# Kernel tuning notes

Measured on AMD Instinct MI355X. Metric: run time of the kernel, lower is better.

## Reference

```python
import jax, jax.numpy as jnp
import numpy as np

B, L, D = 2, 2048, 1024
H = 16
DH = D // H
DFF = 4096
THETA = 10000.0
EPS = 1e-5


def setup_inputs() -> dict:
    key = jax.random.key(0)
    ks = jax.random.split(key, 6)
    s_qkv = (2.0 / (D + 3 * D)) ** 0.5
    s_o = (2.0 / (D + D)) ** 0.5
    s_ff = (2.0 / (D + DFF)) ** 0.5
    return {
        'x': jax.random.normal(ks[0], (B, L, D), jnp.float32),
        'w_qkv': jax.random.normal(ks[1], (3 * D, D), jnp.float32) * s_qkv,
        'w_o': jax.random.normal(ks[2], (D, D), jnp.float32) * s_o,
        'w1': jax.random.normal(ks[3], (DFF, D), jnp.float32) * s_ff,
        'w2': jax.random.normal(ks[4], (D, DFF), jnp.float32) * s_ff,
        'w3': jax.random.normal(ks[5], (DFF, D), jnp.float32) * s_ff,
        'g1': jnp.ones((D,), jnp.float32),
        'g2': jnp.ones((D,), jnp.float32),
    }


def _rmsnorm(x, g):
    xf = x.astype(jnp.float32)
    inv = jax.lax.rsqrt(jnp.mean(xf * xf, axis=-1, keepdims=True) + EPS)
    return (xf * inv * g).astype(x.dtype)


def _rotate_pair(t):
    # interleaved pairs: (x0,x1,x2,x3,...) -> (-x1,x0,-x3,x2,...)
    t2 = t.reshape(t.shape[:-1] + (t.shape[-1] // 2, 2))
    r = jnp.stack((-t2[..., 1], t2[..., 0]), axis=-1)
    return r.reshape(t.shape)


def reference(x, w_qkv, w_o, w1, w2, w3, g1, g2):
    Bb, Ll, Dd = x.shape
    # --- attention sublayer ---
    y = _rmsnorm(x, g1)
    qkv = y @ w_qkv.T                       # (B, L, 3D)
    q, k, v = jnp.split(qkv, 3, axis=-1)
    def to_heads(t):
        return t.reshape(Bb, Ll, H, DH).transpose(0, 2, 1, 3)  # (B,H,L,Dh)
    q, k, v = to_heads(q), to_heads(k), to_heads(v)
    # RoPE (interleaved), positions = 0..L-1
    inv_freq = 1.0 / (THETA ** (jnp.arange(0, DH, 2, dtype=jnp.float32) / DH))
    ang = jnp.arange(Ll, dtype=jnp.float32)[:, None] * inv_freq  # (L, Dh/2)
    ang = jnp.repeat(ang, 2, axis=-1)                            # (L, Dh)
    cos, sin = jnp.cos(ang), jnp.sin(ang)
    q = q * cos + _rotate_pair(q) * sin
    k = k * cos + _rotate_pair(k) * sin
    att = jnp.einsum('bhqd,bhkd->bhqk', q, k) * (1.0 / np.sqrt(DH))
    causal = jnp.tril(jnp.ones((Ll, Ll), dtype=bool))
    att = jnp.where(causal, att, -jnp.inf)
    att = jax.nn.softmax(att, axis=-1)
    yh = jnp.einsum('bhqk,bhkd->bhqd', att, v)
    y = yh.transpose(0, 2, 1, 3).reshape(Bb, Ll, Dd)
    x = x + y @ w_o.T
    # --- SwiGLU FFN sublayer ---
    y = _rmsnorm(x, g2)
    h = jax.nn.silu(y @ w1.T) * (y @ w3.T)
    return x + h @ w2.T
```

## Files before the change

kernel.cpp:

```cpp
#include <hip/hip_runtime.h>


typedef __attribute__((ext_vector_type(8))) short short8;
typedef __attribute__((ext_vector_type(4))) float f32x4;

#define DEV __device__ __forceinline__

DEV unsigned short f2b(float f) {
  unsigned int u = __builtin_bit_cast(unsigned int, f);
  unsigned int r = u + 0x7fffu + ((u >> 16) & 1u);
  return (unsigned short)(r >> 16);
}
DEV float b2f(unsigned short h) {
  return __builtin_bit_cast(float, ((unsigned int)h) << 16);
}
DEV unsigned int cvtpk(float lo, float hi) {
  unsigned int r;
  asm("v_cvt_pk_bf16_f32 %0, %1, %2" : "=v"(r) : "v"(lo), "v"(hi));
  return r;
}
DEV f32x4 MFMA(short8 a, short8 b, f32x4 c) {
  return __builtin_amdgcn_mfma_f32_16x16x32_bf16(a, b, c, 0, 0, 0);
}
DEV void gload16(const void* g, void* lds) {
  __builtin_amdgcn_global_load_lds((const __attribute__((address_space(1))) void*)g,
                                   (__attribute__((address_space(3))) void*)lds, 16, 0, 0);
}

__global__ __launch_bounds__(256) void prep_k(
    const float* __restrict__ wqkv, const float* __restrict__ wo,
    const float* __restrict__ w1, const float* __restrict__ w3,
    const float* __restrict__ w2,
    unsigned short* __restrict__ wqkv_b, unsigned short* __restrict__ wo_b,
    unsigned short* __restrict__ w1_b, unsigned short* __restrict__ w3_b,
    unsigned short* __restrict__ w2_b,
    float2* __restrict__ rtab,
    const float* __restrict__ x, const float* __restrict__ g1,
    unsigned short* __restrict__ yb) {
  const int bid = blockIdx.x;
  const int t = threadIdx.x;
  if (bid < 16384) {
    const float* src;
    unsigned short* dst;
    int base;
    if (bid < 3072) { src = wqkv; dst = wqkv_b; base = bid; }
    else if (bid < 4096) { src = wo; dst = wo_b; base = bid - 3072; }
    else if (bid < 8192) { src = w1; dst = w1_b; base = bid - 4096; }
    else if (bid < 12288) { src = w3; dst = w3_b; base = bid - 8192; }
    else { src = w2; dst = w2_b; base = bid - 12288; }
    const int i = (base * 256 + t) * 4;
    float4 v = *(const float4*)(src + i);
    ushort4 o;
    o.x = f2b(v.x); o.y = f2b(v.y); o.z = f2b(v.z); o.w = f2b(v.w);
    *(ushort4*)(dst + i) = o;
  } else if (bid < 16640) {
    const int i = (bid - 16384) * 256 + t;
    const int lt = i >> 5, pr = i & 31;
    const float invf = __expf((float)pr * -0.28782313662425572f);
    const float ang = (float)lt * invf;
    float sn, cs;
    sincosf(ang, &sn, &cs);
    rtab[i] = make_float2(cs, sn);
  } else {
    const int row = bid - 16640;
    const float4 v = *(const float4*)(x + (size_t)row * 1024 + t * 4);
    float ss = v.x * v.x + v.y * v.y + v.z * v.z + v.w * v.w;
#pragma unroll
    for (int m = 32; m >= 1; m >>= 1) ss += __shfl_xor(ss, m, 64);
    __shared__ float red[4];
    if ((t & 63) == 0) red[t >> 6] = ss;
    __syncthreads();
    float tot = red[0] + red[1] + red[2] + red[3];
    float inv = rsqrtf(tot * (1.0f / 1024.0f) + 1e-5f);
    ushort4 o;
    o.x = f2b(v.x * inv * g1[t * 4 + 0]);
    o.y = f2b(v.y * inv * g1[t * 4 + 1]);
    o.z = f2b(v.z * inv * g1[t * 4 + 2]);
    o.w = f2b(v.w * inv * g1[t * 4 + 3]);
    *(ushort4*)(yb + (size_t)row * 1024 + t * 4) = o;
  }
}

__global__ __launch_bounds__(256) void rms_k(const float* __restrict__ x,
                                             const float* __restrict__ g,
                                             unsigned short* __restrict__ out) {
  const int row = blockIdx.x;
  const int t = threadIdx.x;
  const float4 v = *(const float4*)(x + (size_t)row * 1024 + t * 4);
  float ss = v.x * v.x + v.y * v.y + v.z * v.z + v.w * v.w;
#pragma unroll
  for (int m = 32; m >= 1; m >>= 1) ss += __shfl_xor(ss, m, 64);
  __shared__ float red[4];
  if ((t & 63) == 0) red[t >> 6] = ss;
  __syncthreads();
  float tot = red[0] + red[1] + red[2] + red[3];
  float inv = rsqrtf(tot * (1.0f / 1024.0f) + 1e-5f);
  ushort4 o;
  o.x = f2b(v.x * inv * g[t * 4 + 0]);
  o.y = f2b(v.y * inv * g[t * 4 + 1]);
  o.z = f2b(v.z * inv * g[t * 4 + 2]);
  o.w = f2b(v.w * inv * g[t * 4 + 3]);
  *(ushort4*)(out + (size_t)row * 1024 + t * 4) = o;
}

template <int MODE>
__global__ __launch_bounds__(256, 3) void gemm_bt(
    const unsigned short* __restrict__ A, const unsigned short* __restrict__ B0,
    int M, int N, int K,
    float* __restrict__ outF, const float* __restrict__ resid,
    unsigned short* __restrict__ q, unsigned short* __restrict__ k2,
    unsigned short* __restrict__ v,
    const float2* __restrict__ rtab) {
  __shared__ __align__(16) unsigned short As[2][128 * 32];
  __shared__ __align__(16) unsigned short Bs[2][128 * 32];
  const int t = threadIdx.x;
  const int wv = t >> 6, ln = t & 63;
  const int l15 = ln & 15, grp = ln >> 4;
  const int wr = wv >> 1, wc = wv & 1;
  int m0, n0;
  if constexpr (MODE == 1) {
    const int d = blockIdx.y * 8 + blockIdx.x;
    const int xcd = d & 7, j = d >> 3;
    m0 = (xcd * 4 + (j >> 3)) * 128;
    n0 = (j & 7) * 128;
  } else {
    m0 = blockIdx.y * 128;
    n0 = blockIdx.x * 128;
  }

  const char* sA0 = (const char*)A + ((size_t)(m0 + (t >> 2)) * K + (t & 3) * 8) * 2;
  const char* sA1 = (const char*)A + ((size_t)(m0 + 64 + (t >> 2)) * K + (t & 3) * 8) * 2;
  const char* sB0 = (const char*)B0 + ((size_t)(n0 + (t >> 2)) * K + (t & 3) * 8) * 2;
  const char* sB1 = (const char*)B0 + ((size_t)(n0 + 64 + (t >> 2)) * K + (t & 3) * 8) * 2;

  f32x4 acc[4][4];
#pragma unroll
  for (int mm = 0; mm < 4; ++mm)
#pragma unroll
    for (int nn = 0; nn < 4; ++nn) acc[mm][nn] = (f32x4){0.f, 0.f, 0.f, 0.f};

  const int KT = K >> 5;
  gload16(sA0, (char*)As[0] + wv * 1024);
  gload16(sA1, (char*)As[0] + 4096 + wv * 1024);
  gload16(sB0, (char*)Bs[0] + wv * 1024);
  gload16(sB1, (char*)Bs[0] + 4096 + wv * 1024);

#pragma unroll 1
  for (int kt = 0; kt < KT; ++kt) {
    const int par = kt & 1;
    const size_t ko = (size_t)((kt + 1 < KT) ? (kt + 1) : kt) * 64;
    gload16(sA0 + ko, (char*)As[par ^ 1] + wv * 1024);
    gload16(sA1 + ko, (char*)As[par ^ 1] + 4096 + wv * 1024);
    gload16(sB0 + ko, (char*)Bs[par ^ 1] + wv * 1024);
    gload16(sB1 + ko, (char*)Bs[par ^ 1] + 4096 + wv * 1024);
    asm volatile("s_waitcnt vmcnt(4)" ::: "memory");
    __builtin_amdgcn_s_barrier();
    const unsigned short* Ab = As[par];
    const unsigned short* Bb = Bs[par];
    short8 af[4], bf0[4];
#pragma unroll
    for (int mm = 0; mm < 4; ++mm)
      af[mm] = *(const short8*)&Ab[(wr * 64 + mm * 16 + l15) * 32 + grp * 8];
#pragma unroll
    for (int nn = 0; nn < 4; ++nn)
      bf0[nn] = *(const short8*)&Bb[(wc * 64 + nn * 16 + l15) * 32 + grp * 8];
#pragma unroll
    for (int mm = 0; mm < 4; ++mm)
#pragma unroll
      for (int nn = 0; nn < 4; ++nn) acc[mm][nn] = MFMA(af[mm], bf0[nn], acc[mm][nn]);
    __builtin_amdgcn_s_barrier();
  }

#pragma unroll
  for (int mm = 0; mm < 4; ++mm)
#pragma unroll
    for (int nn = 0; nn < 4; ++nn)
#pragma unroll
      for (int j = 0; j < 4; ++j) {
        const int r = m0 + wr * 64 + mm * 16 + grp * 4 + j;
        const int c = n0 + wc * 64 + nn * 16 + l15;
        float val = acc[mm][nn][j];
        if constexpr (MODE == 0) {
          const int mat = c >> 10;
          const int rem = c & 1023;
          const int hh = rem >> 6;
          const int dh = rem & 63;
          const int bt = r >> 11;
          const int lt = r & 2047;
          float outv = val;
          if (mat < 2) {
            const float partner = __shfl_xor(val, 1, 64);
            const float2 cs = rtab[lt * 32 + (dh >> 1)];
            outv = (dh & 1) ? (val * cs.x + partner * cs.y) : (val * cs.x - partner * cs.y);
          }
          if (mat == 0) outv *= 0.18033688011112042f;
          unsigned short* dst = (mat == 0) ? q : ((mat == 1) ? k2 : v);
          dst[((size_t)(bt * 16 + hh) * 2048 + lt) * 64 + dh] = f2b(outv);
        } else {
          const size_t idx = (size_t)r * N + c;
          outF[idx] = resid[idx] + val;
        }
      }
}

__global__ __launch_bounds__(256, 3) void gemm_sk(
    const unsigned short* __restrict__ A, const unsigned short* __restrict__ B0,
    unsigned short* __restrict__ part) {
  __shared__ __align__(16) unsigned short As[2][128 * 32];
  __shared__ __align__(16) unsigned short Bs[2][128 * 32];
  const int t = threadIdx.x;
  const int wv = t >> 6, ln = t & 63;
  const int l15 = ln & 15, grp = ln >> 4;
  const int wr = wv >> 1, wc = wv & 1;
  const int d = blockIdx.y * 8 + blockIdx.x;
  const int xcd = d & 7, j = d >> 3;
  const int m0 = (xcd * 4 + (j >> 3)) * 128;
  const int n0 = (j & 7) * 128;
  const size_t kbase = (size_t)blockIdx.z * 2048;

  const char* sA0 = (const char*)A + ((size_t)(m0 + (t >> 2)) * 4096 + kbase + (t & 3) * 8) * 2;
  const char* sA1 = (const char*)A + ((size_t)(m0 + 64 + (t >> 2)) * 4096 + kbase + (t & 3) * 8) * 2;
  const char* sB0 = (const char*)B0 + ((size_t)(n0 + (t >> 2)) * 4096 + kbase + (t & 3) * 8) * 2;
  const char* sB1 = (const char*)B0 + ((size_t)(n0 + 64 + (t >> 2)) * 4096 + kbase + (t & 3) * 8) * 2;

  f32x4 acc[4][4];
#pragma unroll
  for (int mm = 0; mm < 4; ++mm)
#pragma unroll
    for (int nn = 0; nn < 4; ++nn) acc[mm][nn] = (f32x4){0.f, 0.f, 0.f, 0.f};

  gload16(sA0, (char*)As[0] + wv * 1024);
  gload16(sA1, (char*)As[0] + 4096 + wv * 1024);
  gload16(sB0, (char*)Bs[0] + wv * 1024);
  gload16(sB1, (char*)Bs[0] + 4096 + wv * 1024);

#pragma unroll 1
  for (int kt = 0; kt < 64; ++kt) {
    const int par = kt & 1;
    const size_t ko = (size_t)((kt + 1 < 64) ? (kt + 1) : kt) * 64;
    gload16(sA0 + ko, (char*)As[par ^ 1] + wv * 1024);
    gload16(sA1 + ko, (char*)As[par ^ 1] + 4096 + wv * 1024);
    gload16(sB0 + ko, (char*)Bs[par ^ 1] + wv * 1024);
    gload16(sB1 + ko, (char*)Bs[par ^ 1] + 4096 + wv * 1024);
    asm volatile("s_waitcnt vmcnt(4)" ::: "memory");
    __builtin_amdgcn_s_barrier();
    const unsigned short* Ab = As[par];
    const unsigned short* Bb = Bs[par];
    short8 af[4], bf0[4];
#pragma unroll
    for (int mm = 0; mm < 4; ++mm)
      af[mm] = *(const short8*)&Ab[(wr * 64 + mm * 16 + l15) * 32 + grp * 8];
#pragma unroll
    for (int nn = 0; nn < 4; ++nn)
      bf0[nn] = *(const short8*)&Bb[(wc * 64 + nn * 16 + l15) * 32 + grp * 8];
#pragma unroll
    for (int mm = 0; mm < 4; ++mm)
#pragma unroll
      for (int nn = 0; nn < 4; ++nn) acc[mm][nn] = MFMA(af[mm], bf0[nn], acc[mm][nn]);
    __builtin_amdgcn_s_barrier();
  }

  unsigned short* pz = part + (size_t)blockIdx.z * 4194304;
#pragma unroll
  for (int mm = 0; mm < 4; ++mm)
#pragma unroll
    for (int nn = 0; nn < 4; ++nn)
#pragma unroll
      for (int j = 0; j < 4; ++j) {
        const int r = m0 + wr * 64 + mm * 16 + grp * 4 + j;
        const int c = n0 + wc * 64 + nn * 16 + l15;
        pz[(size_t)r * 1024 + c] = f2b(acc[mm][nn][j]);
      }
}

__global__ __launch_bounds__(256) void red_k(const float* __restrict__ x2,
                                             const unsigned short* __restrict__ part,
                                             float* __restrict__ out) {
  const int i = (blockIdx.x * 256 + threadIdx.x) * 4;
  float4 r = *(const float4*)(x2 + i);
#pragma unroll
  for (int z = 0; z < 2; ++z) {
    const ushort4 p = *(const ushort4*)(part + (size_t)z * 4194304 + i);
    r.x += b2f(p.x);
    r.y += b2f(p.y);
    r.z += b2f(p.z);
    r.w += b2f(p.w);
  }
  *(float4*)(out + i) = r;
}

__global__ __launch_bounds__(512, 2) void ffn_k(
    const unsigned short* __restrict__ A, const unsigned short* __restrict__ B0,
    const unsigned short* __restrict__ B1, unsigned short* __restrict__ outH) {
  __shared__ __align__(16) char Asm[2][32768];
  __shared__ __align__(16) char Bsm[2][32768];
  const int t = threadIdx.x;
  const int wid = t >> 6, lane = t & 63;
  const int l15 = lane & 15, grp = lane >> 4;
  const int wr = wid >> 2, wc = wid & 3;
  const int d = blockIdx.x;
  const int xcd = d & 7, r8 = d >> 3;
  const int m0 = (r8 >> 2) * 256;
  const int n0 = (xcd * 4 + (r8 & 3)) * 256;

  const char* srcA0;
  const char* srcB0;
  {
    const int lb = t * 16;
    const int r = lb >> 7;
    const int sw = (((lb >> 4) & 7) * 16) ^ ((r & 7) << 4);
    srcA0 = (const char*)A + (size_t)(m0 + r) * 2048 + sw;
    const int R = n0 + r;
    const unsigned short* bsrc = ((R >> 4) & 1) ? B1 : B0;
    const int br = ((R >> 5) << 4) + (R & 15);
    srcB0 = (const char*)bsrc + (size_t)br * 2048 + sw;
  }
  char* const ldsA = (char*)Asm + wid * 1024;
  char* const ldsB = (char*)Bsm + wid * 1024;

  f32x4 acc[8][4];
#pragma unroll
  for (int m = 0; m < 8; ++m)
#pragma unroll
    for (int n = 0; n < 4; ++n) acc[m][n] = (f32x4){0.f, 0.f, 0.f, 0.f};

  gload16(srcA0 + 0 * 131072, ldsA + 0 * 8192);
  gload16(srcA0 + 1 * 131072, ldsA + 1 * 8192);
  gload16(srcB0 + 0 * 65536, ldsB + 0 * 8192);
  gload16(srcB0 + 1 * 65536, ldsB + 1 * 8192);
  gload16(srcB0 + 2 * 65536, ldsB + 2 * 8192);
  gload16(srcB0 + 3 * 65536, ldsB + 3 * 8192);
  gload16(srcA0 + 2 * 131072, ldsA + 2 * 8192);
  gload16(srcA0 + 3 * 131072, ldsA + 3 * 8192);

  const int rA0 = wr * 64 + l15;
  const int rB0 = wc * 32 + l15;

#pragma unroll 1
  for (int kt = 0; kt < 16; ++kt) {
    const int cb = kt & 1;
    const size_t koff = (size_t)((kt + 1 < 16) ? (kt + 1) : kt) * 128;
    const char* Ab = Asm[cb];
    const char* Bb = Bsm[cb];
    const int nb = (cb ^ 1) * 32768;

    short8 a0[2][4], a1[2][4], b0[2][2], b1[2][2];

    gload16(srcA0 + 0 * 131072 + koff, ldsA + nb + 0 * 8192);
    gload16(srcA0 + 1 * 131072 + koff, ldsA + nb + 1 * 8192);
    asm volatile("s_waitcnt vmcnt(4)" ::: "memory");
    __builtin_amdgcn_s_barrier();
#pragma unroll
    for (int ks = 0; ks < 2; ++ks)
#pragma unroll
      for (int m = 0; m < 4; ++m) {
        const int r = rA0 + m * 16;
        a0[ks][m] = *(const short8*)(Ab + r * 128 + ((ks * 64 + grp * 16) ^ ((r & 7) << 4)));
      }
#pragma unroll
    for (int ks = 0; ks < 2; ++ks)
#pragma unroll
      for (int n = 0; n < 2; ++n) {
        const int r = rB0 + n * 16;
        b0[ks][n] = *(const short8*)(Bb + r * 128 + ((ks * 64 + grp * 16) ^ ((r & 7) << 4)));
      }
#pragma unroll
    for (int ks = 0; ks < 2; ++ks)
#pragma unroll
      for (int n = 0; n < 2; ++n) {
        const int r = 128 + rB0 + n * 16;
        b1[ks][n] = *(const short8*)(Bb + r * 128 + ((ks * 64 + grp * 16) ^ ((r & 7) << 4)));
      }
    __builtin_amdgcn_s_setprio(1);
#pragma unroll
    for (int ks = 0; ks < 2; ++ks)
#pragma unroll
      for (int m = 0; m < 4; ++m)
#pragma unroll
        for (int n = 0; n < 2; ++n) acc[m][n] = MFMA(a0[ks][m], b0[ks][n], acc[m][n]);
    __builtin_amdgcn_s_setprio(0);

    gload16(srcB0 + 0 * 65536 + koff, ldsB + nb + 0 * 8192);
    gload16(srcB0 + 1 * 65536 + koff, ldsB + nb + 1 * 8192);
    gload16(srcB0 + 2 * 65536 + koff, ldsB + nb + 2 * 8192);
    gload16(srcB0 + 3 * 65536 + koff, ldsB + nb + 3 * 8192);
    asm volatile("s_waitcnt vmcnt(6)" ::: "memory");
    __builtin_amdgcn_s_barrier();
#pragma unroll
    for (int ks = 0; ks < 2; ++ks)
#pragma unroll
      for (int m = 0; m < 4; ++m) {
        const int r = 128 + rA0 + m * 16;
        a1[ks][m] = *(const short8*)(Ab + r * 128 + ((ks * 64 + grp * 16) ^ ((r & 7) << 4)));
      }
    __builtin_amdgcn_s_setprio(1);
#pragma unroll
    for (int ks = 0; ks < 2; ++ks)
#pragma unroll
      for (int m = 0; m < 4; ++m)
#pragma unroll
        for (int n = 0; n < 2; ++n) acc[m][2 + n] = MFMA(a0[ks][m], b1[ks][n], acc[m][2 + n]);
    __builtin_amdgcn_s_setprio(0);

    gload16(srcA0 + 2 * 131072 + koff, ldsA + nb + 2 * 8192);
    gload16(srcA0 + 3 * 131072 + koff, ldsA + nb + 3 * 8192);
    __builtin_amdgcn_s_barrier();
    __builtin_amdgcn_s_setprio(1);
#pragma unroll
    for (int ks = 0; ks < 2; ++ks)
#pragma unroll
      for (int m = 0; m < 4; ++m)
#pragma unroll
        for (int n = 0; n < 2; ++n) acc[4 + m][2 + n] = MFMA(a1[ks][m], b1[ks][n], acc[4 + m][2 + n]);
    __builtin_amdgcn_s_setprio(0);

    __builtin_amdgcn_s_barrier();
    __builtin_amdgcn_s_setprio(1);
#pragma unroll
    for (int ks = 0; ks < 2; ++ks)
#pragma unroll
      for (int m = 0; m < 4; ++m)
#pragma unroll
        for (int n = 0; n < 2; ++n) acc[4 + m][n] = MFMA(a1[ks][m], b0[ks][n], acc[4 + m][n]);
    __builtin_amdgcn_s_setprio(0);
  }

#pragma unroll
  for (int mh = 0; mh < 2; ++mh)
#pragma unroll
    for (int m = 0; m < 4; ++m)
#pragma unroll
      for (int nh = 0; nh < 2; ++nh)
#pragma unroll
        for (int j = 0; j < 4; ++j) {
          const int row = m0 + mh * 128 + wr * 64 + m * 16 + grp * 4 + j;
          const int ch = (n0 >> 1) + nh * 64 + wc * 16 + l15;
          const float a1v = acc[mh * 4 + m][nh * 2 + 0][j];
          const float a3v = acc[mh * 4 + m][nh * 2 + 1][j];
          const float hval = a1v / (1.0f + __expf(-a1v)) * a3v;
          outH[(size_t)row * 4096 + ch] = f2b(hval);
        }
}

__global__ __launch_bounds__(256) void vtr_k(const unsigned short* __restrict__ v,
                                             unsigned short* __restrict__ vt) {
  __shared__ __align__(16) unsigned short tile[64][72];
  const int bh = blockIdx.y;
  const int lt0 = blockIdx.x * 64;
  const int t = threadIdx.x;
  const int r = t >> 2;
  const int c0 = (t & 3) * 16;
  const unsigned short* src = v + ((size_t)bh * 2048 + lt0 + r) * 64 + c0;
  *(short8*)&tile[r][c0] = *(const short8*)src;
  *(short8*)&tile[r][c0 + 8] = *(const short8*)(src + 8);
  __syncthreads();
  unsigned short outv[16];
#pragma unroll
  for (int i = 0; i < 16; ++i) outv[i] = tile[c0 + i][r];
  unsigned short* dst = vt + ((size_t)bh * 64 + r) * 2048 + lt0 + c0;
  *(short8*)dst = *(short8*)&outv[0];
  *(short8*)(dst + 8) = *(short8*)&outv[8];
}

__global__ __launch_bounds__(256) void attn_k(const unsigned short* __restrict__ qb,
                                              const unsigned short* __restrict__ kb,
                                              const unsigned short* __restrict__ vt,
                                              unsigned short* __restrict__ yh) {
  const int dd = blockIdx.x;
  const int xcd = dd & 7, idx = dd >> 3;
  const int bh = xcd + 8 * (idx & 3);
  const int pair = idx >> 2;
  const int t = threadIdx.x;
  const int w = t >> 6, lane = t & 63;
  const int l15 = lane & 15, grp = lane >> 4;

  __shared__ __align__(16) char Ks[2][8192];
  __shared__ __align__(16) char Vs[2][8192];
  __shared__ __align__(16) char Ps[8192];
  char* Pw = Ps + w * 2048;

  const char* kg = (const char*)kb + (size_t)bh * 262144;
  const char* vg = (const char*)vt + (size_t)bh * 262144;

  const int lb0 = t * 16, lb1 = 4096 + t * 16;
  const int r0 = lb0 >> 7, r1 = lb1 >> 7;
  const int sl0 = (lb0 & 0x70) ^ ((r0 & 7) << 4);
  const int sl1 = (lb1 & 0x70) ^ ((r1 & 7) << 4);
  const char* srcK0 = kg + r0 * 128 + sl0;
  const char* srcK1 = kg + r1 * 128 + sl1;
  const char* srcV0 = vg + (size_t)r0 * 4096 + sl0;
  const char* srcV1 = vg + (size_t)r1 * 4096 + sl1;

  const int bq = bh >> 4, hh = bh & 15;

#pragma unroll 1
  for (int half = 0; half < 2; ++half) {
    const int qblk = half ? pair : (31 - pair);
    const int qw = qblk * 64 + w * 16;

    const unsigned short* qp = qb + ((size_t)bh * 2048 + qw) * 64;
    const short8 qf0 = *(const short8*)(qp + l15 * 64 + grp * 8);
    const short8 qf1 = *(const short8*)(qp + l15 * 64 + 32 + grp * 8);

    f32x4 o[4];
#pragma unroll
    for (int d = 0; d < 4; ++d) o[d] = (f32x4){0.f, 0.f, 0.f, 0.f};
    float mrun = -3.0e38f, lrun = 0.f;

    const int nkt = qblk + 1;

    __syncthreads();
    {
      gload16(srcK0, Ks[0] + w * 1024);
      gload16(srcK1, Ks[0] + 4096 + w * 1024);
      gload16(srcV0, Vs[0] + w * 1024);
      gload16(srcV1, Vs[0] + 4096 + w * 1024);
    }

#pragma unroll 1
    for (int kt = 0; kt < nkt; ++kt) {
      const int par = kt & 1;
      const int ktn = (kt + 1 < nkt) ? (kt + 1) : kt;
      gload16(srcK0 + (size_t)ktn * 8192, Ks[par ^ 1] + w * 1024);
      gload16(srcK1 + (size_t)ktn * 8192, Ks[par ^ 1] + 4096 + w * 1024);
      gload16(srcV0 + ktn * 128, Vs[par ^ 1] + w * 1024);
      gload16(srcV1 + ktn * 128, Vs[par ^ 1] + 4096 + w * 1024);
      asm volatile("s_waitcnt vmcnt(4)" ::: "memory");
      __builtin_amdgcn_s_barrier();

      const char* Kc = Ks[par];
      const char* Vc = Vs[par];

      f32x4 st[4];
#pragma unroll
      for (int c = 0; c < 4; ++c) {
        const int r = c * 16 + l15;
        const int xr = (r & 7) << 4;
        const short8 kf0 = *(const short8*)(Kc + r * 128 + ((grp * 16) ^ xr));
        const short8 kf1 = *(const short8*)(Kc + r * 128 + ((64 + grp * 16) ^ xr));
        f32x4 z = (f32x4){0.f, 0.f, 0.f, 0.f};
        __builtin_amdgcn_s_setprio(1);
        z = MFMA(kf0, qf0, z);
        z = MFMA(kf1, qf1, z);
        __builtin_amdgcn_s_setprio(0);
        st[c] = z;
      }

      const bool diag = (kt == qblk);
      const int qg = qw + l15;
      float av[4][4];
      float tm = -3.0e38f;
#pragma unroll
      for (int c = 0; c < 4; ++c)
#pragma unroll
        for (int j = 0; j < 4; ++j) {
          float x = st[c][j];
          if (diag) {
            const int kg2 = kt * 64 + c * 16 + grp * 4 + j;
            if (kg2 > qg) x = -3.0e38f;
          }
          av[c][j] = x;
          tm = fmaxf(tm, x);
        }
      tm = fmaxf(tm, __shfl_xor(tm, 16, 64));
      tm = fmaxf(tm, __shfl_xor(tm, 32, 64));

      const float mold = mrun;
      const bool need = tm > mold;
      mrun = fmaxf(mold, tm);
      const float aown = need ? __builtin_amdgcn_exp2f(mold - mrun) : 1.0f;
      if (__any(need)) {
        float am[4];
#pragma unroll
        for (int j = 0; j < 4; ++j) am[j] = __shfl(aown, grp * 4 + j, 64);
#pragma unroll
        for (int d = 0; d < 4; ++d)
#pragma unroll
          for (int j = 0; j < 4; ++j) o[d][j] *= am[j];
      }

      float rs = 0.f;
      uint2 pk[4];
#pragma unroll
      for (int c = 0; c < 4; ++c) {
        const float p0 = __builtin_amdgcn_exp2f(av[c][0] - mrun);
        const float p1 = __builtin_amdgcn_exp2f(av[c][1] - mrun);
        const float p2 = __builtin_amdgcn_exp2f(av[c][2] - mrun);
        const float p3 = __builtin_amdgcn_exp2f(av[c][3] - mrun);
        rs += (p0 + p1) + (p2 + p3);
        pk[c].x = cvtpk(p0, p1);
        pk[c].y = cvtpk(p2, p3);
      }
      rs += __shfl_xor(rs, 16, 64);
      rs += __shfl_xor(rs, 32, 64);
      lrun = lrun * aown + rs;

      const int xp = (l15 & 7) << 4;
      char* prow = Pw + l15 * 128;
#pragma unroll
      for (int c = 0; c < 4; ++c)
        *(uint2*)(prow + ((32 * c + 8 * grp) ^ xp)) = pk[c];

      const short8 pa0 = *(const short8*)(prow + ((grp * 16) ^ xp));
      const short8 pa1 = *(const short8*)(prow + ((64 + grp * 16) ^ xp));
#pragma unroll
      for (int db = 0; db < 4; ++db) {
        const int rv = db * 16 + l15;
        const int xv = (rv & 7) << 4;
        const short8 vf0 = *(const short8*)(Vc + rv * 128 + ((grp * 16) ^ xv));
        const short8 vf1 = *(const short8*)(Vc + rv * 128 + ((64 + grp * 16) ^ xv));
        __builtin_amdgcn_s_setprio(1);
        o[db] = MFMA(pa0, vf0, o[db]);
        o[db] = MFMA(pa1, vf1, o[db]);
        __builtin_amdgcn_s_setprio(0);
      }
      __builtin_amdgcn_s_barrier();
    }

    float lr[4];
#pragma unroll
    for (int j = 0; j < 4; ++j) lr[j] = __shfl(lrun, grp * 4 + j, 64);
#pragma unroll
    for (int db = 0; db < 4; ++db)
#pragma unroll
      for (int j = 0; j < 4; ++j) {
        const float valo = o[db][j] / lr[j];
        const size_t rowo = (size_t)bq * 2048 + qw + grp * 4 + j;
        yh[rowo * 1024 + hh * 64 + db * 16 + l15] = f2b(valo);
      }
  }
}

extern "C" void kernel_launch(void* const* d_in, const int* in_sizes, int n_in,
                              void* d_out, int out_size, void* d_ws, size_t ws_size,
                              hipStream_t stream) {
  const float* x = (const float*)d_in[0];
  const float* wqkv = (const float*)d_in[1];
  const float* wo = (const float*)d_in[2];
  const float* w1 = (const float*)d_in[3];
  const float* w2 = (const float*)d_in[4];
  const float* w3 = (const float*)d_in[5];
  const float* g1 = (const float*)d_in[6];
  const float* g2 = (const float*)d_in[7];

  char* ws = (char*)d_ws;
  unsigned short* wqkv_b = (unsigned short*)(ws + 0);
  unsigned short* wo_b = (unsigned short*)(ws + 6291456);
  unsigned short* w1_b = (unsigned short*)(ws + 8388608);
  unsigned short* w3_b = (unsigned short*)(ws + 16777216);
  unsigned short* yb = (unsigned short*)(ws + 25165824);
  float* x2 = (float*)(ws + 33554432);
  float2* rtab = (float2*)(ws + 33554432);
  unsigned short* w2_b = (unsigned short*)(ws + 50331648);
  unsigned short* qb = (unsigned short*)(ws + 58720256);
  unsigned short* kb = (unsigned short*)(ws + 67108864);
  unsigned short* vb = (unsigned short*)(ws + 75497472);
  unsigned short* vt = (unsigned short*)(ws + 83886080);
  unsigned short* yh = vb;
  unsigned short* hb = (unsigned short*)(ws + 58720256);
  unsigned short* part = (unsigned short*)(ws + 0);
  if (ws_size < 92274688) return;

  prep_k<<<20736, 256, 0, stream>>>(wqkv, wo, w1, w3, w2,
                                    wqkv_b, wo_b, w1_b, w3_b, w2_b,
                                    rtab, x, g1, yb);
  gemm_bt<0><<<dim3(24, 32), 256, 0, stream>>>(yb, wqkv_b, 4096, 3072, 1024,
                                               nullptr, nullptr, qb, kb, vb, rtab);
  vtr_k<<<dim3(32, 32), 256, 0, stream>>>(vb, vt);
  attn_k<<<dim3(512), 256, 0, stream>>>(qb, kb, vt, yh);
  gemm_bt<1><<<dim3(8, 32), 256, 0, stream>>>(yh, wo_b, 4096, 1024, 1024,
                                              x2, x, nullptr, nullptr, nullptr, nullptr);
  rms_k<<<4096, 256, 0, stream>>>(x2, g2, yb);
  ffn_k<<<dim3(512), 512, 0, stream>>>(yb, w1_b, w3_b, hb);
  gemm_sk<<<dim3(8, 32, 2), 256, 0, stream>>>(hb, w2_b, part);
  red_k<<<4096, 256, 0, stream>>>(x2, part, (float*)d_out);
}
```

Baseline: 272.0 us.

## Restructure FFN1 GEMM main loop into deeper ping-pong prefetch with unroll-by-two

Rewrites the gate/up GEMM K-loop as two K-tiles per iteration with fixed even and odd LDS buffers. Global-to-LDS loads for the tile two steps ahead are spread across the four MFMA quadrant phases, with more loads in flight (vmcnt 8). The aim is to hide global latency better and remove per-iteration buffer index arithmetic. In exchange it adds barriers around each phase, and the finer-grained buffer reuse raises the risk of synchronisation overhead or LDS write-after-read hazards.

```diff
diff --git a/kernel.cpp b/kernel.cpp
--- a/kernel.cpp
+++ b/kernel.cpp
@@ -332,44 +332,128 @@
   gload16(srcB0 + 3 * 65536, ldsB + 3 * 8192);
   gload16(srcA0 + 2 * 131072, ldsA + 2 * 8192);
   gload16(srcA0 + 3 * 131072, ldsA + 3 * 8192);
+  gload16(srcA0 + 0 * 131072 + 128, ldsA + 32768 + 0 * 8192);
+  gload16(srcA0 + 1 * 131072 + 128, ldsA + 32768 + 1 * 8192);
+  gload16(srcB0 + 0 * 65536 + 128, ldsB + 32768 + 0 * 8192);
+  gload16(srcB0 + 1 * 65536 + 128, ldsB + 32768 + 1 * 8192);
+  gload16(srcB0 + 2 * 65536 + 128, ldsB + 32768 + 2 * 8192);
+  gload16(srcB0 + 3 * 65536 + 128, ldsB + 32768 + 3 * 8192);
 
   const int rA0 = wr * 64 + l15;
   const int rB0 = wc * 32 + l15;
+  const char* const AbE = Asm[0];
+  const char* const BbE = Bsm[0];
+  const char* const AbO = Asm[1];
+  const char* const BbO = Bsm[1];
+
+  short8 a0[2][4], a1[2][4], b0[2][2], b1[2][2];
 
 #pragma unroll 1
-  for (int kt = 0; kt < 16; ++kt) {
-    const int cb = kt & 1;
-    const size_t koff = (size_t)((kt + 1 < 16) ? (kt + 1) : kt) * 128;
-    const char* Ab = Asm[cb];
-    const char* Bb = Bsm[cb];
-    const int nb = (cb ^ 1) * 32768;
-
-    short8 a0[2][4], a1[2][4], b0[2][2], b1[2][2];
-
-    gload16(srcA0 + 0 * 131072 + koff, ldsA + nb + 0 * 8192);
-    gload16(srcA0 + 1 * 131072 + koff, ldsA + nb + 1 * 8192);
-    asm volatile("s_waitcnt vmcnt(4)" ::: "memory");
+  for (int it = 0; it < 8; ++it) {
+    const size_t kO = (size_t)(2 * it + 1) * 128;
+    const int e2 = (2 * it + 2 < 16) ? (2 * it + 2) : 15;
+    const int o2 = (2 * it + 3 < 16) ? (2 * it + 3) : 15;
+    const size_t kE2 = (size_t)e2 * 128;
+    const size_t kO2 = (size_t)o2 * 128;
+
+    gload16(srcA0 + 2 * 131072 + kO, ldsA + 32768 + 2 * 8192);
+    gload16(srcA0 + 3 * 131072 + kO, ldsA + 32768 + 3 * 8192);
+    asm volatile("s_waitcnt vmcnt(8)" ::: "memory");
     __builtin_amdgcn_s_barrier();
 #pragma unroll
     for (int ks = 0; ks < 2; ++ks)
 #pragma unroll
       for (int m = 0; m < 4; ++m) {
         const int r = rA0 + m * 16;
-        a0[ks][m] = *(const short8*)(Ab + r * 128 + ((ks * 64 + grp * 16) ^ ((r & 7) << 4)));
+        a0[ks][m] = *(const short8*)(AbE + r * 128 + ((ks * 64 + grp * 16) ^ ((r & 7) << 4)));
       }
 #pragma unroll
     for (int ks = 0; ks < 2; ++ks)
 #pragma unroll
       for (int n = 0; n < 2; ++n) {
         const int r = rB0 + n * 16;
-        b0[ks][n] = *(const short8*)(Bb + r * 128 + ((ks * 64 + grp * 16) ^ ((r & 7) << 4)));
-      }
+        b0[ks][n] = *(const short8*)(BbE + r * 128 + ((ks * 64 + grp * 16) ^ ((r & 7) << 4)));
+      }
+    __builtin_amdgcn_s_setprio(1);
+#pragma unroll
+    for (int ks = 0; ks < 2; ++ks)
+#pragma unroll
+      for (int m = 0; m < 4; ++m)
+#pragma unroll
+        for (int n = 0; n < 2; ++n) acc[m][n] = MFMA(a0[ks][m], b0[ks][n], acc[m][n]);
+    __builtin_amdgcn_s_setprio(0);
+    __builtin_amdgcn_s_barrier();
+
 #pragma unroll
     for (int ks = 0; ks < 2; ++ks)
 #pragma unroll
       for (int n = 0; n < 2; ++n) {
         const int r = 128 + rB0 + n * 16;
-        b1[ks][n] = *(const short8*)(Bb + r * 128 + ((ks * 64 + grp * 16) ^ ((r & 7) << 4)));
+        b1[ks][n] = *(const short8*)(BbE + r * 128 + ((ks * 64 + grp * 16) ^ ((r & 7) << 4)));
+      }
+    gload16(srcA0 + 0 * 131072 + kE2, ldsA + 0 * 8192);
+    gload16(srcA0 + 1 * 131072 + kE2, ldsA + 1 * 8192);
+    __builtin_amdgcn_s_barrier();
+    __builtin_amdgcn_s_setprio(1);
+#pragma unroll
+    for (int ks = 0; ks < 2; ++ks)
+#pragma unroll
+      for (int m = 0; m < 4; ++m)
+#pragma unroll
+        for (int n = 0; n < 2; ++n) acc[m][2 + n] = MFMA(a0[ks][m], b1[ks][n], acc[m][2 + n]);
+    __builtin_amdgcn_s_setprio(0);
+    __builtin_amdgcn_s_barrier();
+
+#pragma unroll
+    for (int ks = 0; ks < 2; ++ks)
+#pragma unroll
+      for (int m = 0; m < 4; ++m) {
+        const int r = 128 + rA0 + m * 16;
+        a1[ks][m] = *(const short8*)(AbE + r * 128 + ((ks * 64 + grp * 16) ^ ((r & 7) << 4)));
+      }
+    gload16(srcB0 + 0 * 65536 + kE2, ldsB + 0 * 8192);
+    gload16(srcB0 + 1 * 65536 + kE2, ldsB + 1 * 8192);
+    __builtin_amdgcn_s_barrier();
+    __builtin_amdgcn_s_setprio(1);
+#pragma unroll
+    for (int ks = 0; ks < 2; ++ks)
+#pragma unroll
+      for (int m = 0; m < 4; ++m)
+#pragma unroll
+        for (int n = 0; n < 2; ++n) acc[4 + m][2 + n] = MFMA(a1[ks][m], b1[ks][n], acc[4 + m][2 + n]);
+    __builtin_amdgcn_s_setprio(0);
+    __builtin_amdgcn_s_barrier();
+
+    gload16(srcB0 + 2 * 65536 + kE2, ldsB + 2 * 8192);
+    gload16(srcB0 + 3 * 65536 + kE2, ldsB + 3 * 8192);
+    __builtin_amdgcn_s_barrier();
+    __builtin_amdgcn_s_setprio(1);
+#pragma unroll
+    for (int ks = 0; ks < 2; ++ks)
+#pragma unroll
+      for (int m = 0; m < 4; ++m)
+#pragma unroll
+        for (int n = 0; n < 2; ++n) acc[4 + m][n] = MFMA(a1[ks][m], b0[ks][n], acc[4 + m][n]);
+    __builtin_amdgcn_s_setprio(0);
+    __builtin_amdgcn_s_barrier();
+
+    gload16(srcA0 + 2 * 131072 + kE2, ldsA + 2 * 8192);
+    gload16(srcA0 + 3 * 131072 + kE2, ldsA + 3 * 8192);
+    asm volatile("s_waitcnt vmcnt(8)" ::: "memory");
+    __builtin_amdgcn_s_barrier();
+#pragma unroll
+    for (int ks = 0; ks < 2; ++ks)
+#pragma unroll
+      for (int m = 0; m < 4; ++m) {
+        const int r = rA0 + m * 16;
+        a0[ks][m] = *(const short8*)(AbO + r * 128 + ((ks * 64 + grp * 16) ^ ((r & 7) << 4)));
+      }
+#pragma unroll
+    for (int ks = 0; ks < 2; ++ks)
+#pragma unroll
+      for (int n = 0; n < 2; ++n) {
+        const int r = rB0 + n * 16;
+        b0[ks][n] = *(const short8*)(BbO + r * 128 + ((ks * 64 + grp * 16) ^ ((r & 7) << 4)));
       }
     __builtin_amdgcn_s_setprio(1);
 #pragma unroll
@@ -379,31 +463,37 @@
 #pragma unroll
         for (int n = 0; n < 2; ++n) acc[m][n] = MFMA(a0[ks][m], b0[ks][n], acc[m][n]);
     __builtin_amdgcn_s_setprio(0);
-
-    gload16(srcB0 + 0 * 65536 + koff, ldsB + nb + 0 * 8192);
-    gload16(srcB0 + 1 * 65536 + koff, ldsB + nb + 1 * 8192);
-    gload16(srcB0 + 2 * 65536 + koff, ldsB + nb + 2 * 8192);
-    gload16(srcB0 + 3 * 65536 + koff, ldsB + nb + 3 * 8192);
-    asm volatile("s_waitcnt vmcnt(6)" ::: "memory");
-    __builtin_amdgcn_s_barrier();
+    __builtin_amdgcn_s_barrier();
+
+#pragma unroll
+    for (int ks = 0; ks < 2; ++ks)
+#pragma unroll
+      for (int n = 0; n < 2; ++n) {
+        const int r = 128 + rB0 + n * 16;
+        b1[ks][n] = *(const short8*)(BbO + r * 128 + ((ks * 64 + grp * 16) ^ ((r & 7) << 4)));
+      }
+    gload16(srcA0 + 0 * 131072 + kO2, ldsA + 32768 + 0 * 8192);
+    gload16(srcA0 + 1 * 131072 + kO2, ldsA + 32768 + 1 * 8192);
+    __builtin_amdgcn_s_barrier();
+    __builtin_amdgcn_s_setprio(1);
+#pragma unroll
+    for (int ks = 0; ks < 2; ++ks)
+#pragma unroll
+      for (int m = 0; m < 4; ++m)
+#pragma unroll
+        for (int n = 0; n < 2; ++n) acc[m][2 + n] = MFMA(a0[ks][m], b1[ks][n], acc[m][2 + n]);
+    __builtin_amdgcn_s_setprio(0);
+    __builtin_amdgcn_s_barrier();
+
 #pragma unroll
     for (int ks = 0; ks < 2; ++ks)
 #pragma unroll
       for (int m = 0; m < 4; ++m) {
         const int r = 128 + rA0 + m * 16;
-        a1[ks][m] = *(const short8*)(Ab + r * 128 + ((ks * 64 + grp * 16) ^ ((r & 7) << 4)));
-      }
-    __builtin_amdgcn_s_setprio(1);
-#pragma unroll
-    for (int ks = 0; ks < 2; ++ks)
-#pragma unroll
-      for (int m = 0; m < 4; ++m)
-#pragma unroll
-        for (int n = 0; n < 2; ++n) acc[m][2 + n] = MFMA(a0[ks][m], b1[ks][n], acc[m][2 + n]);
-    __builtin_amdgcn_s_setprio(0);
-
-    gload16(srcA0 + 2 * 131072 + koff, ldsA + nb + 2 * 8192);
-    gload16(srcA0 + 3 * 131072 + koff, ldsA + nb + 3 * 8192);
+        a1[ks][m] = *(const short8*)(AbO + r * 128 + ((ks * 64 + grp * 16) ^ ((r & 7) << 4)));
+      }
+    gload16(srcB0 + 0 * 65536 + kO2, ldsB + 32768 + 0 * 8192);
+    gload16(srcB0 + 1 * 65536 + kO2, ldsB + 32768 + 1 * 8192);
     __builtin_amdgcn_s_barrier();
     __builtin_amdgcn_s_setprio(1);
 #pragma unroll
@@ -413,7 +503,10 @@
 #pragma unroll
         for (int n = 0; n < 2; ++n) acc[4 + m][2 + n] = MFMA(a1[ks][m], b1[ks][n], acc[4 + m][2 + n]);
     __builtin_amdgcn_s_setprio(0);
-
+    __builtin_amdgcn_s_barrier();
+
+    gload16(srcB0 + 2 * 65536 + kO2, ldsB + 32768 + 2 * 8192);
+    gload16(srcB0 + 3 * 65536 + kO2, ldsB + 32768 + 3 * 8192);
     __builtin_amdgcn_s_barrier();
     __builtin_amdgcn_s_setprio(1);
 #pragma unroll
@@ -423,6 +516,7 @@
 #pragma unroll
         for (int n = 0; n < 2; ++n) acc[4 + m][n] = MFMA(a1[ks][m], b0[ks][n], acc[4 + m][n]);
     __builtin_amdgcn_s_setprio(0);
+    __builtin_amdgcn_s_barrier();
   }
 
 #pragma unroll
```

After: 273.2 us. Within noise of the previous version (+0.5%).

## Double attention key tile to 128 and XCD-swizzle QKV GEMM grid

Applied to the files above, without the earlier changes.

The attention kernel now processes 128 keys per iteration instead of 64, using larger K/V/P shared-memory buffers and four MFMA k-steps for PV. This halves the number of loop iterations, barriers and online-softmax rescales. The causal mask is applied whenever the tile overlaps the diagonal, which wastes some work at the boundary. Separately, the QKV GEMM uses a 1D grid remapped so that blocks sharing A rows land on the same XCD, aiming for better L2 reuse. The larger LDS footprint may reduce occupancy.

```diff
diff --git a/kernel.cpp b/kernel.cpp
--- a/kernel.cpp
+++ b/kernel.cpp
@@ -124,8 +124,10 @@
     m0 = (xcd * 4 + (j >> 3)) * 128;
     n0 = (j & 7) * 128;
   } else {
-    m0 = blockIdx.y * 128;
-    n0 = blockIdx.x * 128;
+    const int d = blockIdx.x;
+    const int xcd = d & 7, qd = d >> 3;
+    m0 = (xcd + 8 * (qd / 24)) * 128;
+    n0 = (qd % 24) * 128;
   }
 
   const char* sA0 = (const char*)A + ((size_t)(m0 + (t >> 2)) * K + (t & 3) * 8) * 2;
@@ -474,22 +476,26 @@
   const int w = t >> 6, lane = t & 63;
   const int l15 = lane & 15, grp = lane >> 4;
 
-  __shared__ __align__(16) char Ks[2][8192];
-  __shared__ __align__(16) char Vs[2][8192];
-  __shared__ __align__(16) char Ps[8192];
-  char* Pw = Ps + w * 2048;
+  __shared__ __align__(16) char Ks[2][16384];
+  __shared__ __align__(16) char Vs[2][16384];
+  __shared__ __align__(16) char Ps[16384];
+  char* Pw = Ps + w * 4096;
 
   const char* kg = (const char*)kb + (size_t)bh * 262144;
   const char* vg = (const char*)vt + (size_t)bh * 262144;
 
-  const int lb0 = t * 16, lb1 = 4096 + t * 16;
-  const int r0 = lb0 >> 7, r1 = lb1 >> 7;
-  const int sl0 = (lb0 & 0x70) ^ ((r0 & 7) << 4);
-  const int sl1 = (lb1 & 0x70) ^ ((r1 & 7) << 4);
-  const char* srcK0 = kg + r0 * 128 + sl0;
-  const char* srcK1 = kg + r1 * 128 + sl1;
-  const char* srcV0 = vg + (size_t)r0 * 4096 + sl0;
-  const char* srcV1 = vg + (size_t)r1 * 4096 + sl1;
+  const char* srcK[4];
+  const char* srcV[4];
+#pragma unroll
+  for (int s = 0; s < 4; ++s) {
+    const int lb = s * 4096 + t * 16;
+    const int rK = lb >> 7;
+    const int oK = (lb & 0x70) ^ ((rK & 7) << 4);
+    srcK[s] = kg + rK * 128 + oK;
+    const int rV = lb >> 8;
+    const int oV = (lb & 0xF0) ^ ((rV & 7) << 4);
+    srcV[s] = vg + (size_t)rV * 4096 + oV;
+  }
 
   const int bq = bh >> 4, hh = bh & 15;
 
@@ -507,33 +513,33 @@
     for (int d = 0; d < 4; ++d) o[d] = (f32x4){0.f, 0.f, 0.f, 0.f};
     float mrun = -3.0e38f, lrun = 0.f;
 
-    const int nkt = qblk + 1;
+    const int nkt = (qblk + 2) >> 1;
 
     __syncthreads();
-    {
-      gload16(srcK0, Ks[0] + w * 1024);
-      gload16(srcK1, Ks[0] + 4096 + w * 1024);
-      gload16(srcV0, Vs[0] + w * 1024);
-      gload16(srcV1, Vs[0] + 4096 + w * 1024);
+#pragma unroll
+    for (int s = 0; s < 4; ++s) {
+      gload16(srcK[s], Ks[0] + s * 4096 + w * 1024);
+      gload16(srcV[s], Vs[0] + s * 4096 + w * 1024);
     }
 
 #pragma unroll 1
     for (int kt = 0; kt < nkt; ++kt) {
       const int par = kt & 1;
       const int ktn = (kt + 1 < nkt) ? (kt + 1) : kt;
-      gload16(srcK0 + (size_t)ktn * 8192, Ks[par ^ 1] + w * 1024);
-      gload16(srcK1 + (size_t)ktn * 8192, Ks[par ^ 1] + 4096 + w * 1024);
-      gload16(srcV0 + ktn * 128, Vs[par ^ 1] + w * 1024);
-      gload16(srcV1 + ktn * 128, Vs[par ^ 1] + 4096 + w * 1024);
-      asm volatile("s_waitcnt vmcnt(4)" ::: "memory");
+#pragma unroll
+      for (int s = 0; s < 4; ++s) {
+        gload16(srcK[s] + (size_t)ktn * 16384, Ks[par ^ 1] + s * 4096 + w * 1024);
+        gload16(srcV[s] + (size_t)ktn * 256, Vs[par ^ 1] + s * 4096 + w * 1024);
+      }
+      asm volatile("s_waitcnt vmcnt(8)" ::: "memory");
       __builtin_amdgcn_s_barrier();
 
       const char* Kc = Ks[par];
       const char* Vc = Vs[par];
 
-      f32x4 st[4];
-#pragma unroll
-      for (int c = 0; c < 4; ++c) {
+      f32x4 st[8];
+#pragma unroll
+      for (int c = 0; c < 8; ++c) {
         const int r = c * 16 + l15;
         const int xr = (r & 7) << 4;
         const short8 kf0 = *(const short8*)(Kc + r * 128 + ((grp * 16) ^ xr));
@@ -546,20 +552,19 @@
         st[c] = z;
       }
 
-      const bool diag = (kt == qblk);
+      const bool diag = (kt * 128 + 127 > qw);
       const int qg = qw + l15;
-      float av[4][4];
       float tm = -3.0e38f;
 #pragma unroll
-      for (int c = 0; c < 4; ++c)
+      for (int c = 0; c < 8; ++c)
 #pragma unroll
         for (int j = 0; j < 4; ++j) {
           float x = st[c][j];
           if (diag) {
-            const int kg2 = kt * 64 + c * 16 + grp * 4 + j;
+            const int kg2 = kt * 128 + c * 16 + grp * 4 + j;
             if (kg2 > qg) x = -3.0e38f;
           }
-          av[c][j] = x;
+          st[c][j] = x;
           tm = fmaxf(tm, x);
         }
       tm = fmaxf(tm, __shfl_xor(tm, 16, 64));
@@ -580,13 +585,13 @@
       }
 
       float rs = 0.f;
-      uint2 pk[4];
-#pragma unroll
-      for (int c = 0; c < 4; ++c) {
-        const float p0 = __builtin_amdgcn_exp2f(av[c][0] - mrun);
-        const float p1 = __builtin_amdgcn_exp2f(av[c][1] - mrun);
-        const float p2 = __builtin_amdgcn_exp2f(av[c][2] - mrun);
-        const float p3 = __builtin_amdgcn_exp2f(av[c][3] - mrun);
+      uint2 pk[8];
+#pragma unroll
+      for (int c = 0; c < 8; ++c) {
+        const float p0 = __builtin_amdgcn_exp2f(st[c][0] - mrun);
+        const float p1 = __builtin_amdgcn_exp2f(st[c][1] - mrun);
+        const float p2 = __builtin_amdgcn_exp2f(st[c][2] - mrun);
+        const float p3 = __builtin_amdgcn_exp2f(st[c][3] - mrun);
         rs += (p0 + p1) + (p2 + p3);
         pk[c].x = cvtpk(p0, p1);
         pk[c].y = cvtpk(p2, p3);
@@ -596,22 +601,25 @@
       lrun = lrun * aown + rs;
 
       const int xp = (l15 & 7) << 4;
-      char* prow = Pw + l15 * 128;
-#pragma unroll
-      for (int c = 0; c < 4; ++c)
+      char* prow = Pw + l15 * 256;
+#pragma unroll
+      for (int c = 0; c < 8; ++c)
         *(uint2*)(prow + ((32 * c + 8 * grp) ^ xp)) = pk[c];
 
-      const short8 pa0 = *(const short8*)(prow + ((grp * 16) ^ xp));
-      const short8 pa1 = *(const short8*)(prow + ((64 + grp * 16) ^ xp));
+      short8 pa[4];
+#pragma unroll
+      for (int ks = 0; ks < 4; ++ks)
+        pa[ks] = *(const short8*)(prow + ((ks * 64 + grp * 16) ^ xp));
 #pragma unroll
       for (int db = 0; db < 4; ++db) {
         const int rv = db * 16 + l15;
         const int xv = (rv & 7) << 4;
-        const short8 vf0 = *(const short8*)(Vc + rv * 128 + ((grp * 16) ^ xv));
-        const short8 vf1 = *(const short8*)(Vc + rv * 128 + ((64 + grp * 16) ^ xv));
         __builtin_amdgcn_s_setprio(1);
-        o[db] = MFMA(pa0, vf0, o[db]);
-        o[db] = MFMA(pa1, vf1, o[db]);
+#pragma unroll
+        for (int ks = 0; ks < 4; ++ks) {
+          const short8 vf = *(const short8*)(Vc + rv * 256 + ((ks * 64 + grp * 16) ^ xv));
+          o[db] = MFMA(pa[ks], vf, o[db]);
+        }
         __builtin_amdgcn_s_setprio(0);
       }
       __builtin_amdgcn_s_barrier();
@@ -664,8 +672,8 @@
   prep_k<<<20736, 256, 0, stream>>>(wqkv, wo, w1, w3, w2,
                                     wqkv_b, wo_b, w1_b, w3_b, w2_b,
                                     rtab, x, g1, yb);
-  gemm_bt<0><<<dim3(24, 32), 256, 0, stream>>>(yb, wqkv_b, 4096, 3072, 1024,
-                                               nullptr, nullptr, qb, kb, vb, rtab);
+  gemm_bt<0><<<dim3(768), 256, 0, stream>>>(yb, wqkv_b, 4096, 3072, 1024,
+                                            nullptr, nullptr, qb, kb, vb, rtab);
   vtr_k<<<dim3(32, 32), 256, 0, stream>>>(vb, vt);
   attn_k<<<dim3(512), 256, 0, stream>>>(qb, kb, vt, yh);
   gemm_bt<1><<<dim3(8, 32), 256, 0, stream>>>(yh, wo_b, 4096, 1024, 1024,
```

Result: no change. 267.5 us (median of 3 runs) (-1.7%).
